# Performance work log

Hardware: AMD Instinct MI355X
Metric: run time of the kernel (lower is better)

Reference implementation:

```python
import jax, jax.numpy as jnp
import numpy as np

AGENT_RADIUS = 0.2
SAFETY_DIST = 0.1
_ang = np.linspace(0.0, 2.0 * np.pi, 8, endpoint=False)
OBSTACLES = np.stack([10.0 * np.cos(_ang), 10.0 * np.sin(_ang), 0.5 * np.ones(8)], axis=-1).astype(np.float32)  # (x, y, r)


def _qp_solve(p, G, h):
    """Exact solve of: min_z 0.5 z^T z + p^T z  s.t. G z <= h, z in R^2.
    Equivalent to QPFunction with Q=I. Enumerates KKT candidates over active
    sets of size 0, 1, 2 (closed form in 2D) and picks the feasible optimum.
    p: [2], G: [m,2], h: [m]."""
    m = G.shape[0]
    ii, jj = np.triu_indices(m, 1)
    # active set {} -> unconstrained minimizer
    z0 = -p[None, :]                                        # [1,2]
    # active set {i}: z = -p - lam*g_i, g_i.z = h_i
    gg = jnp.sum(G * G, axis=-1)                            # [m]
    lam1 = (-(G @ p) - h) / (gg + 1e-12)
    z1 = -p[None, :] - lam1[:, None] * G                    # [m,2]
    ok1 = lam1 >= -1e-8
    # active set {i,j}: z solves 2x2 system [g_i; g_j] z = [h_i; h_j]
    Gi, Gj = G[ii], G[jj]                                   # [P,2]
    hi, hj = h[ii], h[jj]
    det = Gi[:, 0] * Gj[:, 1] - Gi[:, 1] * Gj[:, 0]
    det_ok = jnp.abs(det) > 1e-9
    ds = jnp.where(det_ok, det, 1.0)
    zx = (hi * Gj[:, 1] - hj * Gi[:, 1]) / ds
    zy = (Gi[:, 0] * hj - Gj[:, 0] * hi) / ds
    z2 = jnp.stack([zx, zy], axis=-1)                       # [P,2]
    r = -(z2 + p[None, :])                                  # A^T lam = r
    lam_i = (Gj[:, 1] * r[:, 0] - Gj[:, 0] * r[:, 1]) / ds
    lam_j = (Gi[:, 0] * r[:, 1] - Gi[:, 1] * r[:, 0]) / ds
    ok2 = det_ok & (lam_i >= -1e-8) & (lam_j >= -1e-8)
    Z = jnp.concatenate([z0, z1, z2], axis=0)               # [K,2]
    ok = jnp.concatenate([jnp.ones((1,), bool), ok1, ok2], axis=0)
    tol = 1e-6 * (1.0 + jnp.abs(h))
    feas = jnp.all(Z @ G.T <= (h + tol)[None, :], axis=-1)  # [K]
    obj = 0.5 * jnp.sum(Z * Z, axis=-1) + Z @ p
    obj = jnp.where(ok & feas, obj, jnp.inf)
    return Z[jnp.argmin(obj)]


def _forward(x, mean, std, W1, b1, W21, b21, W31, b31, W22, b22, W32, b32):
    x0 = x * std + mean                                     # de-normalized state [B,8]
    hid = jax.nn.relu(x @ W1.T + b1)
    x31 = jax.nn.relu(hid @ W21.T + b21) @ W31.T + b31      # reference control p [B,2]
    x32 = 4.0 * jax.nn.sigmoid(jax.nn.relu(hid @ W22.T + b22) @ W32.T + b32)  # CBF penalties [B,2]
    px, py, theta, v = x0[:, 0], x0[:, 1], x0[:, 2], x0[:, 3]
    ox, oy, oth, ov = x0[:, 4], x0[:, 5], x0[:, 6], x0[:, 7]
    st, ct = jnp.sin(theta), jnp.cos(theta)
    vs, vc = v * st, v * ct
    obs = jnp.asarray(OBSTACLES, x.dtype)
    # static obstacle constraints, vectorized over the n_obs obstacles
    dx = px[:, None] - obs[None, :, 0]                      # [B,n_obs]
    dy = py[:, None] - obs[None, :, 1]
    R = AGENT_RADIUS + obs[:, 2] + SAFETY_DIST
    bar = dx * dx + dy * dy - (R * R)[None, :]
    bdot = 2.0 * dx * vc[:, None] + 2.0 * dy * vs[:, None]
    Lf2b = (2.0 * v * v)[:, None]
    u1 = -2.0 * dx * vs[:, None] + 2.0 * dy * vc[:, None]
    u2 = 2.0 * dx * ct[:, None] + 2.0 * dy * st[:, None]
    G_obs = -jnp.stack([u1, u2], axis=-1)                   # [B,n_obs,2]
    s0, s1 = x32[:, 0:1], x32[:, 1:2]
    h_obs = Lf2b + (s0 + s1) * bdot + (s0 * s1) * bar       # [B,n_obs]
    # opponent constraint
    Ro = 2.0 * AGENT_RADIUS + SAFETY_DIST
    dxo, dyo = px - ox, py - oy
    so, co = jnp.sin(oth), jnp.cos(oth)
    bar_o = dxo * dxo + dyo * dyo - Ro * Ro
    bdot_o = 2.0 * dxo * (vc - ov * co) + 2.0 * dyo * (vs - ov * so)
    Lf2b_o = 2.0 * (v * v + ov * ov + 2.0 * v * ov * jnp.cos(theta - oth))
    u1o = -2.0 * dxo * vs + 2.0 * dyo * vc
    u2o = 2.0 * dxo * ct + 2.0 * dyo * st
    G_opp = -jnp.stack([u1o, u2o], axis=-1)[:, None, :]     # [B,1,2]
    h_opp = (Lf2b_o + (x32[:, 0] + x32[:, 1]) * bdot_o + x32[:, 0] * x32[:, 1] * bar_o)[:, None]
    G = jnp.concatenate([G_obs, G_opp], axis=1)             # [B,m,2]
    h = jnp.concatenate([h_obs, h_opp], axis=1)             # [B,m]
    return jax.vmap(_qp_solve)(x31, G, h)                   # [B,2]


def setup_inputs() -> dict:
    key = jax.random.key(0)
    ks = jax.random.split(key, 6)
    B, nF, H1, H2 = 65536, 8, 256, 128

    def lin(k, o, i):
        k1, k2 = jax.random.split(k)
        W = jax.random.normal(k1, (o, i), jnp.float32) / np.float32(np.sqrt(i))
        b = jax.random.normal(k2, (o,), jnp.float32) * 0.01
        return W, b

    W1, b1 = lin(ks[0], H1, nF)
    W21, b21 = lin(ks[1], H2, H1)
    W31, b31 = lin(ks[2], 2, H2)
    W22, b22 = lin(ks[3], H2, H1)
    W32, b32 = lin(ks[4], 2, H2)
    x = jax.random.normal(ks[5], (B, nF), jnp.float32)
    return {"x": x, "mean": jnp.zeros((nF,), jnp.float32), "std": jnp.ones((nF,), jnp.float32),
            "W1": W1, "b1": b1, "W21": W21, "b21": b21, "W31": W31, "b31": b31,
            "W22": W22, "b22": b22, "W32": W32, "b32": b32, "sgn": 1}


def reference(x, mean, std, W1, b1, W21, b21, W31, b31, W22, b22, W32, b32, sgn):
    # sgn==1 / training path -> batched differentiable QP solve
    return _forward(x, mean, std, W1, b1, W21, b21, W31, b31, W22, b22, W32, b32)
```

## Files before the change

### kernel.cpp

```cpp
#include <hip/hip_runtime.h>
#include <hip/hip_bf16.h>
#include <math.h>


typedef unsigned int u32;
typedef unsigned long long u64;
typedef unsigned short u16;
typedef __attribute__((ext_vector_type(8))) short short8;
typedef __attribute__((ext_vector_type(4))) float f32x4;
typedef __attribute__((ext_vector_type(2))) float f32x2;
typedef __attribute__((ext_vector_type(4))) u32 u32x4;

union Frag { short8 v; u32 u[4]; u32x4 q; };

__device__ __forceinline__ u32 packbf(float a, float b) {
    float2 f2; f2.x = a; f2.y = b;
    __hip_bfloat162 h = __float22bfloat162_rn(f2);
    union { __hip_bfloat162 h2; u32 u; } cv; cv.h2 = h;
    return cv.u;
}

__device__ const float OBX[8] = { 10.f, 7.07106781186547524f, 6.123234e-16f, -7.07106781186547524f,
                                 -10.f, -7.07106781186547524f, -1.8369702e-15f, 7.07106781186547524f };
__device__ const float OBY[8] = { 0.f, 7.07106781186547524f, 10.f, 7.07106781186547524f,
                                  1.2246468e-15f, -7.07106781186547524f, -10.f, -7.07106781186547524f };

#define PI0_ 0x2111111100000000ULL
#define PI1_ 0x5544443333322222ULL
#define PI2_ 0x7665ULL
#define PJ0_ 0x3876543287654321ULL
#define PJ1_ 0x7687658765487654ULL
#define PJ2_ 0x8878ULL
__device__ __forceinline__ int unpack4(u64 w0, u64 w1, u64 w2, int t) {
    u64 w = (t < 16) ? w0 : (t < 32) ? w1 : w2;
    return (int)((w >> ((t & 15) * 4)) & 15);
}

__global__ __launch_bounds__(256)
void prep_kernel(const float* __restrict__ W21, const float* __restrict__ W22,
                 u32* __restrict__ ws)
{
    int idx  = blockIdx.x * 256 + threadIdx.x;
    int lane = idx & 63;
    int nt   = (idx >> 6) & 7;
    int ks   = (idx >> 9) & 7;
    int head = idx >> 12;
    const float* W = head ? W22 : W21;
    int n  = nt * 16 + (lane & 15);
    int k0 = ks * 32 + (lane >> 4) * 8;
    const float* s = W + n * 256 + k0;
    u32x4 o;
    o.x = packbf(s[0], s[1]);
    o.y = packbf(s[2], s[3]);
    o.z = packbf(s[4], s[5]);
    o.w = packbf(s[6], s[7]);
    __builtin_nontemporal_store(o, (u32x4*)ws + idx);
}

__global__ __launch_bounds__(256, 1)
void barriernet_kernel(const float* __restrict__ x,
                       const float* __restrict__ meanp,
                       const float* __restrict__ stdp,
                       const float* __restrict__ W1,
                       const float* __restrict__ b1,
                       const float* __restrict__ b21,
                       const float* __restrict__ W31,
                       const float* __restrict__ b31,
                       const float* __restrict__ b22,
                       const float* __restrict__ W32,
                       const float* __restrict__ b32,
                       const u32* __restrict__ wsB,
                       float* __restrict__ out, int Btot)
{
    const int tid  = threadIdx.x;
    const int wave = tid >> 6;
    const int lane = tid & 63;
    const int q    = lane >> 4;
    const int m    = lane & 15;
    const int blockRow = blockIdx.x * 256;

    __shared__ u32x4 stage[8192];
    __shared__ float lds_p[256][4];

    const u32x4* wsB4 = (const u32x4*)wsB;
    #pragma unroll
    for (int i = 0; i < 32; ++i) {
        int fi = i * 256 + tid;
        stage[fi] = wsB4[fi];
    }

    f32x4 xa[4], xb[4];
    #pragma unroll
    for (int mt = 0; mt < 4; ++mt) {
        int R0 = blockRow + wave * 64 + mt * 16 + m;
        const f32x4* xv = (const f32x4*)(x + (R0 < Btot ? R0 : 0) * 8);
        xa[mt] = xv[0]; xb[mt] = xv[1];
    }

    const f32x4* W1v = (const f32x4*)W1;
    const f32x4* b1v = (const f32x4*)b1;

    Frag A[4][8];
    #pragma unroll
    for (int ks = 0; ks < 8; ++ks) {
        int kb = ks * 32 + q * 8;
        f32x4 bA = b1v[kb >> 2];
        f32x4 bB = b1v[(kb >> 2) + 1];
        float h[4][8];
        #pragma unroll
        for (int j = 0; j < 8; ++j) {
            f32x4 wa = W1v[(kb + j) * 2];
            f32x4 wb = W1v[(kb + j) * 2 + 1];
            float bj = (j < 4) ? bA[j] : bB[j - 4];
            #pragma unroll
            for (int mt = 0; mt < 4; ++mt) {
                float a0 = bj;
                a0 = fmaf(wa.x, xa[mt].x, a0);
                a0 = fmaf(wa.y, xa[mt].y, a0);
                a0 = fmaf(wa.z, xa[mt].z, a0);
                a0 = fmaf(wa.w, xa[mt].w, a0);
                a0 = fmaf(wb.x, xb[mt].x, a0);
                a0 = fmaf(wb.y, xb[mt].y, a0);
                a0 = fmaf(wb.z, xb[mt].z, a0);
                a0 = fmaf(wb.w, xb[mt].w, a0);
                h[mt][j] = fmaxf(a0, 0.f);
            }
        }
        #pragma unroll
        for (int mt = 0; mt < 4; ++mt)
            #pragma unroll
            for (int t = 0; t < 4; ++t)
                A[mt][ks].u[t] = packbf(h[mt][2 * t], h[mt][2 * t + 1]);
    }

    __syncthreads();

    #pragma unroll 1
    for (int head = 0; head < 2; ++head) {
        const float* b2 = head ? b22 : b21;
        const float* W3 = head ? W32 : W31;
        const float* b3 = head ? b32 : b31;

        f32x4 acc[4][8];
        #pragma unroll
        for (int mt = 0; mt < 4; ++mt)
            #pragma unroll
            for (int nt = 0; nt < 8; ++nt) acc[mt][nt] = (f32x4){0.f, 0.f, 0.f, 0.f};

        #pragma unroll
        for (int ks = 0; ks < 8; ++ks) {
            Frag Bf[8];
            #pragma unroll
            for (int nt = 0; nt < 8; ++nt)
                Bf[nt].q = stage[head * 4096 + ks * 512 + nt * 64 + lane];
            #pragma unroll
            for (int nt = 0; nt < 8; ++nt) {
                #pragma unroll
                for (int mt = 0; mt < 4; ++mt)
                    acc[mt][nt] = __builtin_amdgcn_mfma_f32_16x16x32_bf16(
                        A[mt][ks].v, Bf[nt].v, acc[mt][nt], 0, 0, 0);
            }
        }

        float pr0[4][4], pr1[4][4];
        #pragma unroll
        for (int mt = 0; mt < 4; ++mt)
            #pragma unroll
            for (int rg = 0; rg < 4; ++rg) { pr0[mt][rg] = 0.f; pr1[mt][rg] = 0.f; }
        #pragma unroll
        for (int nt = 0; nt < 8; ++nt) {
            int col = nt * 16 + m;
            float b2c = b2[col];
            float w0c = W3[col];
            float w1c = W3[128 + col];
            #pragma unroll
            for (int mt = 0; mt < 4; ++mt) {
                #pragma unroll
                for (int rg = 0; rg < 4; ++rg) {
                    float rv = fmaxf(acc[mt][nt][rg] + b2c, 0.f);
                    pr0[mt][rg] = fmaf(rv, w0c, pr0[mt][rg]);
                    pr1[mt][rg] = fmaf(rv, w1c, pr1[mt][rg]);
                }
            }
        }
        #pragma unroll
        for (int mt = 0; mt < 4; ++mt) {
            #pragma unroll
            for (int rg = 0; rg < 4; ++rg) {
                float v0 = pr0[mt][rg], v1 = pr1[mt][rg];
                #pragma unroll
                for (int off = 1; off < 16; off <<= 1) {
                    v0 += __shfl_xor(v0, off, 64);
                    v1 += __shfl_xor(v1, off, 64);
                }
                pr0[mt][rg] = v0; pr1[mt][rg] = v1;
            }
        }
        if (m == 0) {
            #pragma unroll
            for (int mt = 0; mt < 4; ++mt) {
                #pragma unroll
                for (int rg = 0; rg < 4; ++rg) {
                    int row = wave * 64 + mt * 16 + q * 4 + rg;
                    float a0 = pr0[mt][rg] + b3[0];
                    float a1 = pr1[mt][rg] + b3[1];
                    if (head == 0) {
                        lds_p[row][0] = a0;
                        lds_p[row][1] = a1;
                    } else {
                        lds_p[row][2] = 4.f / (1.f + __expf(-a0));
                        lds_p[row][3] = 4.f / (1.f + __expf(-a1));
                    }
                }
            }
        }
    }
    __syncthreads();

    f32x4 (*qC)[256] = (f32x4(*)[256])stage;

    const int R = blockRow + tid;
    float p0 = lds_p[tid][0];
    float p1 = lds_p[tid][1];
    {
        float s0 = lds_p[tid][2];
        float s1 = lds_p[tid][3];
        float xr[8];
        const float* xp = x + (R < Btot ? R : 0) * 8;
        #pragma unroll
        for (int c = 0; c < 8; ++c) xr[c] = fmaf(xp[c], stdp[c], meanp[c]);
        float px = xr[0], py = xr[1], th = xr[2], v = xr[3];
        float ox = xr[4], oy = xr[5], oth = xr[6], ov = xr[7];
        float st = __sinf(th),  ct = __cosf(th);
        float so = __sinf(oth), co = __cosf(oth);
        float vs = v * st, vc = v * ct;
        float sps = s0 + s1, ss = s0 * s1;
        float Lf2b = 2.f * v * v;
        #pragma unroll 1
        for (int k = 0; k < 8; ++k) {
            float dx = px - OBX[k], dy = py - OBY[k];
            float bar  = dx * dx + dy * dy - 0.64f;
            float bdot = 2.f * dx * vc + 2.f * dy * vs;
            float gx = 2.f * dx * vs - 2.f * dy * vc;
            float gy = -(2.f * dx * ct + 2.f * dy * st);
            float hk = Lf2b + sps * bdot + ss * bar;
            float ht = hk + 1e-6f * (1.f + fabsf(hk));
            qC[k][tid] = (f32x4){gx, gy, hk, ht};
        }
        {
            float dxo = px - ox, dyo = py - oy;
            float bar_o  = dxo * dxo + dyo * dyo - 0.25f;
            float bdot_o = 2.f * dxo * (vc - ov * co) + 2.f * dyo * (vs - ov * so);
            float Lf2b_o = 2.f * (v * v + ov * ov + 2.f * v * ov * __cosf(th - oth));
            float gx = 2.f * dxo * vs - 2.f * dyo * vc;
            float gy = -(2.f * dxo * ct + 2.f * dyo * st);
            float hk = Lf2b_o + sps * bdot_o + ss * bar_o;
            float ht = hk + 1e-6f * (1.f + fabsf(hk));
            qC[8][tid] = (f32x4){gx, gy, hk, ht};
        }
    }
    const f32x4 C0 = qC[0][tid], C1 = qC[1][tid], C2 = qC[2][tid];
    const f32x4 C3 = qC[3][tid], C4 = qC[4][tid], C5 = qC[5][tid];
    const f32x4 C6 = qC[6][tid], C7 = qC[7][tid], C8 = qC[8][tid];

    float bobj = INFINITY;
    float bzx = -p0, bzy = -p1;
    #pragma unroll 2
    for (int c = 0; c < 46; ++c) {
        float zx, zy;
        bool pre;
        if (c == 0) {
            zx = -p0; zy = -p1; pre = true;
        } else if (c <= 9) {
            f32x4 g = qC[c - 1][tid];
            float gg  = g.x * g.x + g.y * g.y;
            float lam = (-(g.x * p0 + g.y * p1) - g.z) / (gg + 1e-12f);
            zx = -p0 - lam * g.x;
            zy = -p1 - lam * g.y;
            pre = (lam >= -1e-8f);
        } else {
            int t = c - 10;
            int pi = unpack4(PI0_, PI1_, PI2_, t);
            int pj = unpack4(PJ0_, PJ1_, PJ2_, t);
            f32x4 gi = qC[pi][tid];
            f32x4 gj = qC[pj][tid];
            float det = gi.x * gj.y - gi.y * gj.x;
            bool dok = fabsf(det) > 1e-9f;
            float ds = dok ? det : 1.0f;
            float inv = 1.0f / ds;
            zx = (gi.z * gj.y - gj.z * gi.y) * inv;
            zy = (gi.x * gj.z - gj.x * gi.z) * inv;
            float rx = -(zx + p0), ry = -(zy + p1);
            float li = (gj.y * rx - gj.x * ry) * inv;
            float lj = (gi.x * ry - gi.y * rx) * inv;
            pre = dok && (li >= -1e-8f) && (lj >= -1e-8f);
        }
        bool ok = pre;
        ok = ok && (zx * C0.x + zy * C0.y <= C0.w);
        ok = ok && (zx * C1.x + zy * C1.y <= C1.w);
        ok = ok && (zx * C2.x + zy * C2.y <= C2.w);
        ok = ok && (zx * C3.x + zy * C3.y <= C3.w);
        ok = ok && (zx * C4.x + zy * C4.y <= C4.w);
        ok = ok && (zx * C5.x + zy * C5.y <= C5.w);
        ok = ok && (zx * C6.x + zy * C6.y <= C6.w);
        ok = ok && (zx * C7.x + zy * C7.y <= C7.w);
        ok = ok && (zx * C8.x + zy * C8.y <= C8.w);
        float obj = 0.5f * (zx * zx + zy * zy) + zx * p0 + zy * p1;
        if (ok && obj < bobj) { bobj = obj; bzx = zx; bzy = zy; }
    }

    if (R < Btot) {
        f32x2 o2; o2.x = bzx; o2.y = bzy;
        ((f32x2*)out)[R] = o2;
    }
}

extern "C" void kernel_launch(void* const* d_in, const int* in_sizes, int n_in,
                              void* d_out, int out_size, void* d_ws, size_t ws_size,
                              hipStream_t stream) {
    const float* x    = (const float*)d_in[0];
    const float* mean = (const float*)d_in[1];
    const float* stdv = (const float*)d_in[2];
    const float* W1   = (const float*)d_in[3];
    const float* b1   = (const float*)d_in[4];
    const float* W21  = (const float*)d_in[5];
    const float* b21  = (const float*)d_in[6];
    const float* W31  = (const float*)d_in[7];
    const float* b31  = (const float*)d_in[8];
    const float* W22  = (const float*)d_in[9];
    const float* b22  = (const float*)d_in[10];
    const float* W32  = (const float*)d_in[11];
    const float* b32  = (const float*)d_in[12];
    int B = in_sizes[0] / 8;
    float* out = (float*)d_out;
    u32* ws = (u32*)d_ws;

    hipLaunchKernelGGL(prep_kernel, dim3(32), dim3(256), 0, stream, W21, W22, ws);

    hipLaunchKernelGGL(barriernet_kernel, dim3((B + 255) / 256), dim3(256), 0, stream,
                       x, mean, stdv, W1, b1, b21, W31, b31, b22, W32, b32,
                       ws, out, B);
}
```

Measured before the change: 120.0 us.

## Compute first layer with bf16 MFMA and LDS transpose instead of scalar FMAs

```diff
diff --git a/kernel.cpp b/kernel.cpp
--- a/kernel.cpp
+++ b/kernel.cpp
@@ -18,6 +18,11 @@
     __hip_bfloat162 h = __float22bfloat162_rn(f2);
     union { __hip_bfloat162 h2; u32 u; } cv; cv.h2 = h;
     return cv.u;
+}
+__device__ __forceinline__ u16 f2bf1(float f) {
+    union { float f; u32 i; } v; v.f = f;
+    u32 b = v.i;
+    return (u16)((b + 0x7fffu + ((b >> 16) & 1u)) >> 16);
 }
 
 __device__ const float OBX[8] = { 10.f, 7.07106781186547524f, 6.123234e-16f, -7.07106781186547524f,
@@ -82,57 +87,68 @@
     __shared__ u32x4 stage[8192];
     __shared__ float lds_p[256][4];
 
+    Frag w1f[16];
+    #pragma unroll
+    for (int nt = 0; nt < 16; ++nt) {
+        if (q == 0) {
+            const f32x4* wv = (const f32x4*)(W1 + (nt * 16 + m) * 8);
+            f32x4 w0 = wv[0], w1 = wv[1];
+            w1f[nt].u[0] = packbf(w0.x, w0.y);
+            w1f[nt].u[1] = packbf(w0.z, w0.w);
+            w1f[nt].u[2] = packbf(w1.x, w1.y);
+            w1f[nt].u[3] = packbf(w1.z, w1.w);
+        } else {
+            w1f[nt].u[0] = 0; w1f[nt].u[1] = 0; w1f[nt].u[2] = 0; w1f[nt].u[3] = 0;
+        }
+    }
+    float b1c[16];
+    #pragma unroll
+    for (int nt = 0; nt < 16; ++nt) b1c[nt] = b1[nt * 16 + m];
+
+    Frag xf[4];
+    #pragma unroll
+    for (int mt = 0; mt < 4; ++mt) {
+        if (q == 0) {
+            int R0 = blockRow + wave * 64 + mt * 16 + m;
+            const f32x4* xv = (const f32x4*)(x + (R0 < Btot ? R0 : 0) * 8);
+            f32x4 x0 = xv[0], x1 = xv[1];
+            xf[mt].u[0] = packbf(x0.x, x0.y);
+            xf[mt].u[1] = packbf(x0.z, x0.w);
+            xf[mt].u[2] = packbf(x1.x, x1.y);
+            xf[mt].u[3] = packbf(x1.z, x1.w);
+        } else {
+            xf[mt].u[0] = 0; xf[mt].u[1] = 0; xf[mt].u[2] = 0; xf[mt].u[3] = 0;
+        }
+    }
+
+    u16* hidw = (u16*)stage + wave * (16 * 264);
+    Frag A[4][8];
+    #pragma unroll
+    for (int mt = 0; mt < 4; ++mt) {
+        #pragma unroll
+        for (int nt = 0; nt < 16; ++nt) {
+            f32x4 c = __builtin_amdgcn_mfma_f32_16x16x32_bf16(
+                xf[mt].v, w1f[nt].v, (f32x4){0.f, 0.f, 0.f, 0.f}, 0, 0, 0);
+            #pragma unroll
+            for (int rg = 0; rg < 4; ++rg) {
+                float v = fmaxf(c[rg] + b1c[nt], 0.f);
+                hidw[(q * 4 + rg) * 264 + nt * 16 + m] = f2bf1(v);
+            }
+        }
+        asm volatile("s_waitcnt lgkmcnt(0)" ::: "memory");
+        #pragma unroll
+        for (int ks = 0; ks < 8; ++ks)
+            A[mt][ks].q = *(const u32x4*)(hidw + m * 264 + ks * 32 + q * 8);
+        asm volatile("s_waitcnt lgkmcnt(0)" ::: "memory");
+    }
+    __syncthreads();
+
     const u32x4* wsB4 = (const u32x4*)wsB;
     #pragma unroll
     for (int i = 0; i < 32; ++i) {
         int fi = i * 256 + tid;
         stage[fi] = wsB4[fi];
     }
-
-    f32x4 xa[4], xb[4];
-    #pragma unroll
-    for (int mt = 0; mt < 4; ++mt) {
-        int R0 = blockRow + wave * 64 + mt * 16 + m;
-        const f32x4* xv = (const f32x4*)(x + (R0 < Btot ? R0 : 0) * 8);
-        xa[mt] = xv[0]; xb[mt] = xv[1];
-    }
-
-    const f32x4* W1v = (const f32x4*)W1;
-    const f32x4* b1v = (const f32x4*)b1;
-
-    Frag A[4][8];
-    #pragma unroll
-    for (int ks = 0; ks < 8; ++ks) {
-        int kb = ks * 32 + q * 8;
-        f32x4 bA = b1v[kb >> 2];
-        f32x4 bB = b1v[(kb >> 2) + 1];
-        float h[4][8];
-        #pragma unroll
-        for (int j = 0; j < 8; ++j) {
-            f32x4 wa = W1v[(kb + j) * 2];
-            f32x4 wb = W1v[(kb + j) * 2 + 1];
-            float bj = (j < 4) ? bA[j] : bB[j - 4];
-            #pragma unroll
-            for (int mt = 0; mt < 4; ++mt) {
-                float a0 = bj;
-                a0 = fmaf(wa.x, xa[mt].x, a0);
-                a0 = fmaf(wa.y, xa[mt].y, a0);
-                a0 = fmaf(wa.z, xa[mt].z, a0);
-                a0 = fmaf(wa.w, xa[mt].w, a0);
-                a0 = fmaf(wb.x, xb[mt].x, a0);
-                a0 = fmaf(wb.y, xb[mt].y, a0);
-                a0 = fmaf(wb.z, xb[mt].z, a0);
-                a0 = fmaf(wb.w, xb[mt].w, a0);
-                h[mt][j] = fmaxf(a0, 0.f);
-            }
-        }
-        #pragma unroll
-        for (int mt = 0; mt < 4; ++mt)
-            #pragma unroll
-            for (int t = 0; t < 4; ++t)
-                A[mt][ks].u[t] = packbf(h[mt][2 * t], h[mt][2 * t + 1]);
-    }
-
     __syncthreads();
 
     #pragma unroll 1
```

Result: slower. 122.9 us (+2.5%).
